# Kernel tuning notes

Measured on AMD Instinct MI355X. Metric: run time of the kernel, lower is better.

Reference implementation:

```python
import jax, jax.numpy as jnp
import numpy as np

B, S, D_IN, Z, D_OUT = 4, 2048, 4096, 1024, 4096
LN_EPS = 1e-5


def _ln(h, g, b):
    # LayerNorm over last axis (matches nn.LayerNorm(z_size))
    m = jnp.mean(h, axis=-1, keepdims=True)
    v = jnp.var(h, axis=-1, keepdims=True)
    return (h - m) * jax.lax.rsqrt(v + LN_EPS) * g + b


def setup_inputs() -> dict:
    key = jax.random.key(0)
    ks = jax.random.split(key, 8)
    s = 0.02  # init_weights uniform range
    return {
        "x": jax.random.normal(ks[0], (B, S, D_IN), jnp.float32),
        "epsilon": jax.random.normal(ks[1], (B, S, Z), jnp.float32),
        "W1": jax.random.uniform(ks[2], (Z, D_IN), jnp.float32, -s, s),
        "b1": jnp.zeros((Z,), jnp.float32),
        "g1": jnp.ones((Z,), jnp.float32),
        "be1": jnp.zeros((Z,), jnp.float32),
        "W2": jax.random.uniform(ks[3], (Z, Z), jnp.float32, -s, s),
        "b2": jnp.zeros((Z,), jnp.float32),
        "g2": jnp.ones((Z,), jnp.float32),
        "be2": jnp.zeros((Z,), jnp.float32),
        "Wmu": jax.random.uniform(ks[4], (Z, Z), jnp.float32, -s, s),
        "bmu": jnp.zeros((Z,), jnp.float32),
        "Wls": jax.random.uniform(ks[5], (Z, Z), jnp.float32, -s, s),
        "bls": jnp.zeros((Z,), jnp.float32),
        "Wzw": jax.random.uniform(ks[6], (D_OUT, D_OUT + Z), jnp.float32, -s, s),
        "bzw": jnp.zeros((D_OUT,), jnp.float32),
    }


def reference(x, epsilon, W1, b1, g1, be1, W2, b2, g2, be2,
              Wmu, bmu, Wls, bls, Wzw, bzw):
    # fc: Linear -> LayerNorm -> Tanh, twice
    h = jnp.tanh(_ln(jnp.einsum('bsd,zd->bsz', x, W1) + b1, g1, be1))
    h = jnp.tanh(_ln(jnp.einsum('bsz,yz->bsy', h, W2) + b2, g2, be2))
    mu = jnp.einsum('bsz,yz->bsy', h, Wmu) + bmu
    logsigma = jnp.einsum('bsz,yz->bsy', h, Wls) + bls
    std = jnp.exp(0.5 * logsigma)
    z = epsilon * std + mu                    # reparameterization
    z = jnp.concatenate([z, x], axis=2)       # [B,S,Z+D_IN]
    out = jnp.einsum('bsc,oc->bso', jnp.tanh(z), Wzw) + bzw
    return (out, mu, std)
```

## Files before the change

### kernel.cpp

```cpp
#include <hip/hip_runtime.h>
#include <cstdint>

typedef unsigned short u16;
typedef __bf16 bf16x8 __attribute__((ext_vector_type(8)));
typedef float f32x4 __attribute__((ext_vector_type(4)));

#define M_TOT 8192
#define D_IN  4096
#define Z_DIM 1024
#define D_OUT 4096
#define K_CAT 5120

struct alignas(8) u16x4 { u16 x, y, z, w; };

__device__ __forceinline__ u16 to_bf16(float f) {
    union { float f; uint32_t u; } v; v.f = f;
    uint32_t u = v.u;
    uint32_t r = (u + 0x7FFFu + ((u >> 16) & 1u)) >> 16;
    return (u16)r;
}

__device__ __forceinline__ void async_load16(const void* g, void* l) {
    __builtin_amdgcn_global_load_lds(
        (const __attribute__((address_space(1))) void*)g,
        (__attribute__((address_space(3))) void*)l,
        16, 0, 0);
}

__global__ __launch_bounds__(256)
void gemm_bt(const u16* __restrict__ A,
             const u16* __restrict__ Bw0, const u16* __restrict__ Bw1,
             const float* __restrict__ bias0, const float* __restrict__ bias1,
             float* __restrict__ C0, float* __restrict__ C1,
             int M, int N, int K)
{
    const u16*  Bw   = blockIdx.z ? Bw1   : Bw0;
    const float* bias = blockIdx.z ? bias1 : bias0;
    float*       C    = blockIdx.z ? C1    : C0;

    __shared__ u16 As[128 * 32];
    __shared__ u16 Bs[128 * 32];

    const int tid  = threadIdx.x;
    const int wave = tid >> 6;
    const int lane = tid & 63;
    const int m0 = blockIdx.y * 128;
    const int n0 = blockIdx.x * 128;
    const int wm = (wave & 1) * 64;
    const int wn = (wave >> 1) * 64;

    const int srow = wave * 32 + (lane >> 2);
    const int scol = (((lane & 3) ^ ((srow >> 1) & 3))) * 8;
    const long long a_off = (long long)(m0 + srow) * K + scol;
    const long long b_off = (long long)(n0 + srow) * K + scol;

    const int fr = lane & 15;
    const int fq = lane >> 4;
    const int rc = (fq ^ ((fr >> 1) & 3)) * 8;

    f32x4 acc[4][4] = {};

    for (int k0 = 0; k0 < K; k0 += 32) {
        async_load16(A  + a_off + k0,            &As[(wave * 32 +  0) * 32]);
        async_load16(A  + a_off + k0 + 16LL * K, &As[(wave * 32 + 16) * 32]);
        async_load16(Bw + b_off + k0,            &Bs[(wave * 32 +  0) * 32]);
        async_load16(Bw + b_off + k0 + 16LL * K, &Bs[(wave * 32 + 16) * 32]);
        __syncthreads();

        bf16x8 af[4], bf[4];
        #pragma unroll
        for (int i = 0; i < 4; i++)
            af[i] = *(const bf16x8*)&As[(wm + i * 16 + fr) * 32 + rc];
        #pragma unroll
        for (int i = 0; i < 4; i++)
            bf[i] = *(const bf16x8*)&Bs[(wn + i * 16 + fr) * 32 + rc];

        #pragma unroll
        for (int mi = 0; mi < 4; mi++)
            #pragma unroll
            for (int ni = 0; ni < 4; ni++)
                acc[mi][ni] = __builtin_amdgcn_mfma_f32_16x16x32_bf16(
                    af[mi], bf[ni], acc[mi][ni], 0, 0, 0);
        __syncthreads();
    }

    #pragma unroll
    for (int ni = 0; ni < 4; ni++) {
        const int col = n0 + wn + ni * 16 + fr;
        const float bv = bias[col];
        #pragma unroll
        for (int mi = 0; mi < 4; mi++) {
            const int row = m0 + wm + mi * 16 + fq * 4;
            float* cp = C + (long long)row * N + col;
            #pragma unroll
            for (int r = 0; r < 4; r++)
                cp[(long long)r * N] = acc[mi][ni][r] + bv;
        }
    }
}


#define BAR() do { asm volatile("" ::: "memory"); \
                   __builtin_amdgcn_s_barrier(); \
                   asm volatile("" ::: "memory"); } while (0)

#define STAGE_A(buf, h, kt_) do { if ((kt_) < nt) {                            \
    const u16* g_ = Ag + (long long)(h) * hstep + ((long long)(kt_) << 6);     \
    async_load16(g_,      &lds16[(buf) * 32768 + (h) * 8192        + wave * 512]); \
    async_load16(g_ + 32, &lds16[(buf) * 32768 + (h) * 8192 + 4096 + wave * 512]); \
  } } while (0)

#define STAGE_B(buf, h, kt_) do { if ((kt_) < nt) {                            \
    const u16* g_ = Bg + (long long)(h) * hstep + ((long long)(kt_) << 6);     \
    async_load16(g_,      &lds16[16384 + (buf) * 32768 + (h) * 8192        + wave * 512]); \
    async_load16(g_ + 32, &lds16[16384 + (buf) * 32768 + (h) * 8192 + 4096 + wave * 512]); \
  } } while (0)

#define LOAD_AF(buf, mbase)                                                    \
    _Pragma("unroll")                                                          \
    for (int mi_ = 0; mi_ < 4; ++mi_) {                                        \
      _Pragma("unroll")                                                        \
      for (int ks_ = 0; ks_ < 2; ++ks_)                                        \
        af[mi_][ks_] = *(const bf16x8*)&lds16[(buf) * 32768 + a_rd             \
                                              + ks_ * 4096 + ((mbase) + mi_) * 512]; \
    }

#define LOAD_B(dst, buf, nbase)                                                \
    _Pragma("unroll")                                                          \
    for (int ni_ = 0; ni_ < 2; ++ni_) {                                        \
      _Pragma("unroll")                                                        \
      for (int ks_ = 0; ks_ < 2; ++ks_)                                        \
        dst[ni_][ks_] = *(const bf16x8*)&lds16[(buf) * 32768 + b_rd            \
                                               + ks_ * 4096 + ((nbase) + ni_) * 512]; \
    }

#define MMA_Q(bfx, mo, no) do {                                                \
    __builtin_amdgcn_s_setprio(1);                                             \
    _Pragma("unroll")                                                          \
    for (int mi_ = 0; mi_ < 4; ++mi_) {                                        \
      _Pragma("unroll")                                                        \
      for (int ni_ = 0; ni_ < 2; ++ni_) {                                      \
        _Pragma("unroll")                                                      \
        for (int ks_ = 0; ks_ < 2; ++ks_)                                      \
          acc[(mo) + mi_][(no) + ni_] = __builtin_amdgcn_mfma_f32_16x16x32_bf16( \
              af[mi_][ks_], bfx[ni_][ks_], acc[(mo) + mi_][(no) + ni_], 0, 0, 0); \
      }                                                                        \
    }                                                                          \
    __builtin_amdgcn_s_setprio(0);                                             \
  } while (0)

#define TILE(b, kt_) do {                                                      \
                                            \
    LOAD_AF(b, 0);                                                             \
    LOAD_B(bf0, b, 0);                                                         \
    STAGE_A((b) ^ 1, 0, (kt_) + 1);                                            \
    BAR();                                                                     \
    MMA_Q(bf0, 0, 0);                                                          \
    BAR();                                                                     \
                                            \
    LOAD_B(bf1, b, 2);                                                         \
    STAGE_A((b) ^ 1, 1, (kt_) + 1);                                            \
    BAR();                                                                     \
    MMA_Q(bf1, 0, 2);                                                          \
    BAR();                                                                     \
     \
    LOAD_AF(b, 4);                                                             \
    STAGE_B(b, 0, (kt_) + 2);                                                  \
    BAR();                                                                     \
    MMA_Q(bf0, 4, 0);                                                          \
    BAR();                                                                     \
                                      \
    STAGE_B(b, 1, (kt_) + 2);                                                  \
    if ((kt_) + 2 < nt) { asm volatile("s_waitcnt vmcnt(4)" ::: "memory"); }   \
    else                { asm volatile("s_waitcnt vmcnt(0)" ::: "memory"); }   \
    BAR();                                                                     \
    MMA_Q(bf1, 4, 2);                                                          \
    BAR();                                                                     \
  } while (0)

__global__ __launch_bounds__(512)
void gemm256(const u16* __restrict__ A,
             const u16* __restrict__ Bw0, const u16* __restrict__ Bw1,
             const float* __restrict__ bias0, const float* __restrict__ bias1,
             float* __restrict__ C0, float* __restrict__ C1,
             int M, int N, int K)
{
    const u16*   Bw   = blockIdx.z ? Bw1   : Bw0;
    const float* bias = blockIdx.z ? bias1 : bias0;
    float*       C    = blockIdx.z ? C1    : C0;

    __shared__ u16 lds16[65536];

    const int tid  = threadIdx.x;
    const int wave = tid >> 6;
    const int lane = tid & 63;
    const int fr   = lane & 15;
    const int fq   = lane >> 4;
    const int wm   = (wave >> 2) * 128;
    const int wn   = (wave & 3) * 64;

    const int nwg  = (int)(gridDim.x * gridDim.y);
    const int bid0 = (int)(blockIdx.y * gridDim.x + blockIdx.x);
    const int bid  = (bid0 & 7) * (nwg >> 3) + (bid0 >> 3);
    const int n0   = (bid % (int)gridDim.x) * 256;
    const int m0   = (bid / (int)gridDim.x) * 256;

    const int nt = K >> 6;

    const int csrc = (tid & 3) ^ ((tid >> 4) & 2);
    const u16* Ag = A  + (long long)(m0 + (tid >> 2)) * K + csrc * 8;
    const u16* Bg = Bw + (long long)(n0 + (tid >> 2)) * K + csrc * 8;
    const long long hstep = 128LL * K;

    const int swz  = (fq * 8) ^ ((fr & 8) << 1);
    const int a_rd = (wave >> 2) * 8192 + fr * 32 + swz;
    const int b_rd = 16384 + ((wave & 3) >> 1) * 8192
                   + ((wave & 1) * 64 + fr) * 32 + swz;

    f32x4 acc[8][4] = {};
    bf16x8 af[4][2], bf0[2][2], bf1[2][2];

    STAGE_B(0, 0, 0);
    STAGE_B(0, 1, 0);
    STAGE_A(0, 0, 0);
    STAGE_A(0, 1, 0);
    STAGE_B(1, 0, 1);
    STAGE_B(1, 1, 1);
    asm volatile("s_waitcnt vmcnt(4)" ::: "memory");
    BAR();

    #pragma unroll 1
    for (int kt = 0; kt < nt; kt += 2) {
        TILE(0, kt);
        TILE(1, kt + 1);
    }

    #pragma unroll
    for (int ni = 0; ni < 4; ++ni) {
        const int col = n0 + wn + ni * 16 + fr;
        const float bv = bias[col];
        #pragma unroll
        for (int mi = 0; mi < 8; ++mi) {
            const int row = m0 + wm + mi * 16 + fq * 4;
            float* cp = C + (long long)row * N + col;
            #pragma unroll
            for (int r = 0; r < 4; ++r)
                cp[(long long)r * N] = acc[mi][ni][r] + bv;
        }
    }
}

#undef BAR
#undef STAGE_A
#undef STAGE_B
#undef LOAD_AF
#undef LOAD_B
#undef MMA_Q
#undef TILE

__global__ __launch_bounds__(256)
void ln_tanh_kernel(const float* __restrict__ in, const float* __restrict__ g,
                    const float* __restrict__ be, u16* __restrict__ out)
{
    const int row = blockIdx.x;
    const int t = threadIdx.x;
    const float4 v = ((const float4*)(in + (long long)row * 1024))[t];
    float s  = v.x + v.y + v.z + v.w;
    float s2 = v.x * v.x + v.y * v.y + v.z * v.z + v.w * v.w;
    #pragma unroll
    for (int off = 32; off > 0; off >>= 1) {
        s  += __shfl_down(s,  off);
        s2 += __shfl_down(s2, off);
    }
    __shared__ float red[8];
    if ((t & 63) == 0) { red[t >> 6] = s; red[4 + (t >> 6)] = s2; }
    __syncthreads();
    s  = red[0] + red[1] + red[2] + red[3];
    s2 = red[4] + red[5] + red[6] + red[7];
    const float mean = s * (1.0f / 1024.0f);
    const float inv  = rsqrtf(s2 * (1.0f / 1024.0f) - mean * mean + 1e-5f);
    const float4 gg = ((const float4*)g)[t];
    const float4 bb = ((const float4*)be)[t];
    u16x4 o;
    o.x = to_bf16(tanhf((v.x - mean) * inv * gg.x + bb.x));
    o.y = to_bf16(tanhf((v.y - mean) * inv * gg.y + bb.y));
    o.z = to_bf16(tanhf((v.z - mean) * inv * gg.z + bb.z));
    o.w = to_bf16(tanhf((v.w - mean) * inv * gg.w + bb.w));
    ((u16x4*)(out + (long long)row * 1024))[t] = o;
}

__global__ __launch_bounds__(256)
void prep_x_kernel(const float* __restrict__ x, u16* __restrict__ xb,
                   u16* __restrict__ zc)
{
    const long long i = (long long)blockIdx.x * 256 + threadIdx.x;
    const float4 v = ((const float4*)x)[i];
    u16x4 b;
    b.x = to_bf16(v.x); b.y = to_bf16(v.y); b.z = to_bf16(v.z); b.w = to_bf16(v.w);
    ((u16x4*)xb)[i] = b;
    const long long flat = i * 4;
    const long long row = flat >> 12;
    const int col = (int)(flat & 4095);
    u16x4 tq;
    tq.x = to_bf16(tanhf(v.x)); tq.y = to_bf16(tanhf(v.y));
    tq.z = to_bf16(tanhf(v.z)); tq.w = to_bf16(tanhf(v.w));
    *(u16x4*)(zc + row * (long long)K_CAT + 1024 + col) = tq;
}

__global__ __launch_bounds__(256)
void reparam_kernel(const float* __restrict__ mu, float* __restrict__ lsstd,
                    const float* __restrict__ eps, u16* __restrict__ zc)
{
    const long long row = blockIdx.x;
    const int c = threadIdx.x * 4;
    const long long idx = row * 1024 + c;
    const float4 m = *(const float4*)(mu + idx);
    const float4 l = *(const float4*)(lsstd + idx);
    const float4 e = *(const float4*)(eps + idx);
    float4 sd;
    sd.x = expf(0.5f * l.x); sd.y = expf(0.5f * l.y);
    sd.z = expf(0.5f * l.z); sd.w = expf(0.5f * l.w);
    *(float4*)(lsstd + idx) = sd;
    u16x4 t;
    t.x = to_bf16(tanhf(e.x * sd.x + m.x));
    t.y = to_bf16(tanhf(e.y * sd.y + m.y));
    t.z = to_bf16(tanhf(e.z * sd.z + m.z));
    t.w = to_bf16(tanhf(e.w * sd.w + m.w));
    *(u16x4*)(zc + row * (long long)K_CAT + c) = t;
}

__global__ __launch_bounds__(256)
void cvt_kernel(const float* __restrict__ src, u16* __restrict__ dst, long long n4)
{
    const long long i = (long long)blockIdx.x * 256 + threadIdx.x;
    if (i >= n4) return;
    const float4 v = ((const float4*)src)[i];
    u16x4 b;
    b.x = to_bf16(v.x); b.y = to_bf16(v.y); b.z = to_bf16(v.z); b.w = to_bf16(v.w);
    ((u16x4*)dst)[i] = b;
}

__global__ __launch_bounds__(256)
void cvt4_kernel(const float* __restrict__ s0, u16* __restrict__ d0,
                 const float* __restrict__ s1, u16* __restrict__ d1,
                 const float* __restrict__ s2, u16* __restrict__ d2,
                 const float* __restrict__ s3, u16* __restrict__ d3)
{
    long long i = (long long)blockIdx.x * 256 + threadIdx.x;
    const float* s; u16* d;
    if (i < 1048576)      { s = s0; d = d0; }
    else if (i < 1310720) { s = s1; d = d1; i -= 1048576; }
    else if (i < 1572864) { s = s2; d = d2; i -= 1310720; }
    else                  { s = s3; d = d3; i -= 1572864; }
    const float4 v = ((const float4*)s)[i];
    u16x4 b;
    b.x = to_bf16(v.x); b.y = to_bf16(v.y); b.z = to_bf16(v.z); b.w = to_bf16(v.w);
    ((u16x4*)d)[i] = b;
}

extern "C" void kernel_launch(void* const* d_in, const int* in_sizes, int n_in,
                              void* d_out, int out_size, void* d_ws, size_t ws_size,
                              hipStream_t stream)
{
    const float* x   = (const float*)d_in[0];
    const float* eps = (const float*)d_in[1];
    const float* W1  = (const float*)d_in[2];
    const float* b1  = (const float*)d_in[3];
    const float* g1  = (const float*)d_in[4];
    const float* be1 = (const float*)d_in[5];
    const float* W2  = (const float*)d_in[6];
    const float* b2  = (const float*)d_in[7];
    const float* g2  = (const float*)d_in[8];
    const float* be2 = (const float*)d_in[9];
    const float* Wmu = (const float*)d_in[10];
    const float* bmu = (const float*)d_in[11];
    const float* Wls = (const float*)d_in[12];
    const float* bls = (const float*)d_in[13];
    const float* Wzw = (const float*)d_in[14];
    const float* bzw = (const float*)d_in[15];

    float* out  = (float*)d_out;
    float* mu   = out + (long long)M_TOT * D_OUT;
    float* std_ = mu  + (long long)M_TOT * Z_DIM;

    char* ws = (char*)d_ws;
    u16*   xb   = (u16*)(ws);
    u16*   zc   = (u16*)(ws +  67108864);
    u16*   h1   = (u16*)(ws + 150994944);
    u16*   h2   = (u16*)(ws + 167772160);
    float* pre  = (float*)(ws + 184549376);
    u16*   W1b  = (u16*)(ws + 218103808);
    u16*   W2b  = (u16*)(ws + 226492416);
    u16*   Wmub = (u16*)(ws + 228589568);
    u16*   Wlsb = (u16*)(ws + 230686720);
    u16*   Wzwb = (u16*)(ws);

    cvt4_kernel<<<7168, 256, 0, stream>>>(W1, W1b, W2, W2b, Wmu, Wmub, Wls, Wlsb);

    prep_x_kernel<<<32768, 256, 0, stream>>>(x, xb, zc);

    gemm_bt<<<dim3(8, 64, 1), 256, 0, stream>>>(xb, W1b, W1b, b1, b1, pre, pre,
                                                M_TOT, Z_DIM, D_IN);
    ln_tanh_kernel<<<8192, 256, 0, stream>>>(pre, g1, be1, h1);

    cvt_kernel<<<20480, 256, 0, stream>>>(Wzw, Wzwb, 5242880);

    gemm_bt<<<dim3(8, 64, 1), 256, 0, stream>>>(h1, W2b, W2b, b2, b2, pre, pre,
                                                M_TOT, Z_DIM, Z_DIM);
    ln_tanh_kernel<<<8192, 256, 0, stream>>>(pre, g2, be2, h2);

    gemm256<<<dim3(4, 32, 2), 512, 0, stream>>>(h2, Wmub, Wlsb, bmu, bls, mu, std_,
                                                M_TOT, Z_DIM, Z_DIM);

    reparam_kernel<<<8192, 256, 0, stream>>>(mu, std_, eps, zc);

    gemm256<<<dim3(16, 32, 1), 512, 0, stream>>>(zc, Wzwb, Wzwb, bzw, bzw, out, out,
                                                 M_TOT, D_OUT, K_CAT);
}
```

Measured before the change: 930.7 us.

## Restructure GEMM main loop into k-split register pipeline with fewer barriers

Reorganises the inner tile of the 256x256 GEMM so each step splits K into two halves. Per wave it loads 4 A fragments and 4 B fragments and issues 16 MFMAs per group, and it prefetches the next tile's first fragments before the last MMA group. Barriers drop from eight per tile to two. Global-to-LDS staging for both A and B now targets the other buffer one tile ahead, replacing the previous B-two-tiles-ahead scheme, and waits with vmcnt(0). This cuts barrier stalls and LDS read latency exposure, but it uses more fragment registers and shortens the global prefetch distance.

```diff
diff --git a/kernel.cpp b/kernel.cpp
--- a/kernel.cpp
+++ b/kernel.cpp
@@ -116,65 +116,53 @@
     async_load16(g_ + 32, &lds16[16384 + (buf) * 32768 + (h) * 8192 + 4096 + wave * 512]); \
   } } while (0)
 
-#define LOAD_AF(buf, mbase)                                                    \
+#define R_AF(dst, buf, mbase, ks)                                              \
     _Pragma("unroll")                                                          \
-    for (int mi_ = 0; mi_ < 4; ++mi_) {                                        \
-      _Pragma("unroll")                                                        \
-      for (int ks_ = 0; ks_ < 2; ++ks_)                                        \
-        af[mi_][ks_] = *(const bf16x8*)&lds16[(buf) * 32768 + a_rd             \
-                                              + ks_ * 4096 + ((mbase) + mi_) * 512]; \
-    }
-
-#define LOAD_B(dst, buf, nbase)                                                \
+    for (int mi_ = 0; mi_ < 4; ++mi_)                                          \
+      dst[mi_] = *(const bf16x8*)&lds16[(buf) * 32768 + a_rd                   \
+                                        + (ks) * 4096 + ((mbase) + mi_) * 512];
+
+#define R_BF(dst, buf, ks)                                                     \
     _Pragma("unroll")                                                          \
-    for (int ni_ = 0; ni_ < 2; ++ni_) {                                        \
-      _Pragma("unroll")                                                        \
-      for (int ks_ = 0; ks_ < 2; ++ks_)                                        \
-        dst[ni_][ks_] = *(const bf16x8*)&lds16[(buf) * 32768 + b_rd            \
-                                               + ks_ * 4096 + ((nbase) + ni_) * 512]; \
-    }
-
-#define MMA_Q(bfx, mo, no) do {                                                \
+    for (int ni_ = 0; ni_ < 4; ++ni_)                                          \
+      dst[ni_] = *(const bf16x8*)&lds16[(buf) * 32768 + b_rd                   \
+                                        + (ks) * 4096 + ni_ * 512];
+
+#define MMA16(mo, afv, bfv) do {                                               \
     __builtin_amdgcn_s_setprio(1);                                             \
     _Pragma("unroll")                                                          \
     for (int mi_ = 0; mi_ < 4; ++mi_) {                                        \
       _Pragma("unroll")                                                        \
-      for (int ni_ = 0; ni_ < 2; ++ni_) {                                      \
-        _Pragma("unroll")                                                      \
-        for (int ks_ = 0; ks_ < 2; ++ks_)                                      \
-          acc[(mo) + mi_][(no) + ni_] = __builtin_amdgcn_mfma_f32_16x16x32_bf16( \
-              af[mi_][ks_], bfx[ni_][ks_], acc[(mo) + mi_][(no) + ni_], 0, 0, 0); \
-      }                                                                        \
+      for (int ni_ = 0; ni_ < 4; ++ni_)                                        \
+        acc[(mo) + mi_][ni_] = __builtin_amdgcn_mfma_f32_16x16x32_bf16(        \
+            afv[mi_], bfv[ni_], acc[(mo) + mi_][ni_], 0, 0, 0);                \
     }                                                                          \
     __builtin_amdgcn_s_setprio(0);                                             \
   } while (0)
 
 #define TILE(b, kt_) do {                                                      \
-                                            \
-    LOAD_AF(b, 0);                                                             \
-    LOAD_B(bf0, b, 0);                                                         \
+                       \
+    R_AF(afB, b, 4, 0);                                                        \
     STAGE_A((b) ^ 1, 0, (kt_) + 1);                                            \
+    STAGE_A((b) ^ 1, 1, (kt_) + 1);                                            \
+    MMA16(0, afA, bfA);                                                        \
+                \
+    R_AF(afC, b, 0, 1);                                                        \
+    R_BF(bfB, b, 1);                                                           \
+    STAGE_B((b) ^ 1, 0, (kt_) + 1);                                            \
+    STAGE_B((b) ^ 1, 1, (kt_) + 1);                                            \
+    MMA16(4, afB, bfA);                                                        \
+            \
+    R_AF(afD, b, 4, 1);                                                        \
+    MMA16(0, afC, bfB);                                                        \
+    asm volatile("s_waitcnt vmcnt(0)" ::: "memory");                           \
     BAR();                                                                     \
-    MMA_Q(bf0, 0, 0);                                                          \
-    BAR();                                                                     \
-                                            \
-    LOAD_B(bf1, b, 2);                                                         \
-    STAGE_A((b) ^ 1, 1, (kt_) + 1);                                            \
-    BAR();                                                                     \
-    MMA_Q(bf1, 0, 2);                                                          \
-    BAR();                                                                     \
-     \
-    LOAD_AF(b, 4);                                                             \
-    STAGE_B(b, 0, (kt_) + 2);                                                  \
-    BAR();                                                                     \
-    MMA_Q(bf0, 4, 0);                                                          \
-    BAR();                                                                     \
-                                      \
-    STAGE_B(b, 1, (kt_) + 2);                                                  \
-    if ((kt_) + 2 < nt) { asm volatile("s_waitcnt vmcnt(4)" ::: "memory"); }   \
-    else                { asm volatile("s_waitcnt vmcnt(0)" ::: "memory"); }   \
-    BAR();                                                                     \
-    MMA_Q(bf1, 4, 2);                                                          \
+            \
+    if ((kt_) + 1 < nt) {                                                      \
+      R_AF(afA, (b) ^ 1, 0, 0);                                                \
+      R_BF(bfA, (b) ^ 1, 0);                                                   \
+    }                                                                          \
+    MMA16(4, afD, bfB);                                                        \
     BAR();                                                                     \
   } while (0)
 
@@ -218,16 +206,16 @@
                    + ((wave & 1) * 64 + fr) * 32 + swz;
 
     f32x4 acc[8][4] = {};
-    bf16x8 af[4][2], bf0[2][2], bf1[2][2];
-
+    bf16x8 afA[4], afB[4], afC[4], afD[4], bfA[4], bfB[4];
+
+    STAGE_A(0, 0, 0);
+    STAGE_A(0, 1, 0);
     STAGE_B(0, 0, 0);
     STAGE_B(0, 1, 0);
-    STAGE_A(0, 0, 0);
-    STAGE_A(0, 1, 0);
-    STAGE_B(1, 0, 1);
-    STAGE_B(1, 1, 1);
-    asm volatile("s_waitcnt vmcnt(4)" ::: "memory");
+    asm volatile("s_waitcnt vmcnt(0)" ::: "memory");
     BAR();
+    R_AF(afA, 0, 0, 0);
+    R_BF(bfA, 0, 0);
 
     #pragma unroll 1
     for (int kt = 0; kt < nt; kt += 2) {
@@ -253,9 +241,9 @@
 #undef BAR
 #undef STAGE_A
 #undef STAGE_B
-#undef LOAD_AF
-#undef LOAD_B
-#undef MMA_Q
+#undef R_AF
+#undef R_BF
+#undef MMA16
 #undef TILE
 
 __global__ __launch_bounds__(256)
```

Result: slower. 1.153 ms (+23.9%).

## Switch gemm256 to 32x32x16 MFMA and fuse exp into logsigma epilogue

Applied to the files above, without the earlier changes.

Rewrites the 256x256 GEMM inner loop to use 32x32x16 bf16 MFMA tiles instead of 16x16x32. The LDS fragment reads, swizzle and register layout change to match, and the B fragments for the next tile are prefetched across iterations. The larger instruction should give more math per LDS read and fewer instructions per tile. The exp(0.5*x) for std moves into the GEMM epilogue, so reparam no longer reads and rewrites that buffer. The new LDS read pattern may cause bank conflicts, and the epilogue stores become strided by row.

```diff
diff --git a/kernel.cpp b/kernel.cpp
--- a/kernel.cpp
+++ b/kernel.cpp
@@ -4,6 +4,7 @@
 typedef unsigned short u16;
 typedef __bf16 bf16x8 __attribute__((ext_vector_type(8)));
 typedef float f32x4 __attribute__((ext_vector_type(4)));
+typedef float f32x16 __attribute__((ext_vector_type(16)));
 
 #define M_TOT 8192
 #define D_IN  4096
@@ -116,65 +117,67 @@
     async_load16(g_ + 32, &lds16[16384 + (buf) * 32768 + (h) * 8192 + 4096 + wave * 512]); \
   } } while (0)
 
-#define LOAD_AF(buf, mbase)                                                    \
+#define R32A(dst, buf, mp, sp)                                                 \
     _Pragma("unroll")                                                          \
-    for (int mi_ = 0; mi_ < 4; ++mi_) {                                        \
+    for (int mi_ = 0; mi_ < 2; ++mi_) {                                        \
       _Pragma("unroll")                                                        \
-      for (int ks_ = 0; ks_ < 2; ++ks_)                                        \
-        af[mi_][ks_] = *(const bf16x8*)&lds16[(buf) * 32768 + a_rd             \
-                                              + ks_ * 4096 + ((mbase) + mi_) * 512]; \
-    }
-
-#define LOAD_B(dst, buf, nbase)                                                \
+      for (int si_ = 0; si_ < 2; ++si_)                                        \
+        dst[mi_][si_] = *(const bf16x8*)&lds16[(buf) * 32768 + a_rd            \
+            + (sp) * 4096 + ((mp) * 2 + mi_) * 1024 + (si_ ^ rb) * 16];        \
+    }
+
+#define R32B(dst, buf, sp)                                                     \
     _Pragma("unroll")                                                          \
     for (int ni_ = 0; ni_ < 2; ++ni_) {                                        \
       _Pragma("unroll")                                                        \
-      for (int ks_ = 0; ks_ < 2; ++ks_)                                        \
-        dst[ni_][ks_] = *(const bf16x8*)&lds16[(buf) * 32768 + b_rd            \
-                                               + ks_ * 4096 + ((nbase) + ni_) * 512]; \
-    }
-
-#define MMA_Q(bfx, mo, no) do {                                                \
+      for (int si_ = 0; si_ < 2; ++si_)                                        \
+        dst[ni_][si_] = *(const bf16x8*)&lds16[(buf) * 32768 + b_rd            \
+            + (sp) * 4096 + ni_ * 1024 + (si_ ^ rb) * 16];                     \
+    }
+
+#define MMA32(mp, afv, bfv) do {                                               \
     __builtin_amdgcn_s_setprio(1);                                             \
     _Pragma("unroll")                                                          \
-    for (int mi_ = 0; mi_ < 4; ++mi_) {                                        \
+    for (int si_ = 0; si_ < 2; ++si_) {                                        \
       _Pragma("unroll")                                                        \
-      for (int ni_ = 0; ni_ < 2; ++ni_) {                                      \
+      for (int mi_ = 0; mi_ < 2; ++mi_) {                                      \
         _Pragma("unroll")                                                      \
-        for (int ks_ = 0; ks_ < 2; ++ks_)                                      \
-          acc[(mo) + mi_][(no) + ni_] = __builtin_amdgcn_mfma_f32_16x16x32_bf16( \
-              af[mi_][ks_], bfx[ni_][ks_], acc[(mo) + mi_][(no) + ni_], 0, 0, 0); \
+        for (int ni_ = 0; ni_ < 2; ++ni_)                                      \
+          acc[(mp) * 2 + mi_][ni_] = __builtin_amdgcn_mfma_f32_32x32x16_bf16(  \
+              afv[mi_][si_], bfv[ni_][si_], acc[(mp) * 2 + mi_][ni_], 0, 0, 0);\
       }                                                                        \
     }                                                                          \
     __builtin_amdgcn_s_setprio(0);                                             \
   } while (0)
 
 #define TILE(b, kt_) do {                                                      \
-                                            \
-    LOAD_AF(b, 0);                                                             \
-    LOAD_B(bf0, b, 0);                                                         \
+                               \
+    R32A(afE, b, 0, 0);                                                        \
     STAGE_A((b) ^ 1, 0, (kt_) + 1);                                            \
     BAR();                                                                     \
-    MMA_Q(bf0, 0, 0);                                                          \
-    BAR();                                                                     \
-                                            \
-    LOAD_B(bf1, b, 2);                                                         \
+    MMA32(0, afE, bf01);                                                       \
+    BAR();                                                                     \
+         \
+    R32A(afO, b, 1, 0);                                                        \
+    R32B(bf23, b, 1);                                                          \
     STAGE_A((b) ^ 1, 1, (kt_) + 1);                                            \
     BAR();                                                                     \
-    MMA_Q(bf1, 0, 2);                                                          \
-    BAR();                                                                     \
-     \
-    LOAD_AF(b, 4);                                                             \
+    MMA32(1, afO, bf01);                                                       \
+    BAR();                                                                     \
+                          \
+    R32A(afE, b, 0, 1);                                                        \
     STAGE_B(b, 0, (kt_) + 2);                                                  \
     BAR();                                                                     \
-    MMA_Q(bf0, 4, 0);                                                          \
-    BAR();                                                                     \
-                                      \
+    MMA32(0, afE, bf23);                                                       \
+    BAR();                                                                     \
+            \
+    R32A(afO, b, 1, 1);                                                        \
     STAGE_B(b, 1, (kt_) + 2);                                                  \
     if ((kt_) + 2 < nt) { asm volatile("s_waitcnt vmcnt(4)" ::: "memory"); }   \
     else                { asm volatile("s_waitcnt vmcnt(0)" ::: "memory"); }   \
     BAR();                                                                     \
-    MMA_Q(bf1, 4, 2);                                                          \
+    R32B(bf01, (b) ^ 1, 0);                                                    \
+    MMA32(1, afO, bf23);                                                       \
     BAR();                                                                     \
   } while (0)
 
@@ -183,19 +186,21 @@
              const u16* __restrict__ Bw0, const u16* __restrict__ Bw1,
              const float* __restrict__ bias0, const float* __restrict__ bias1,
              float* __restrict__ C0, float* __restrict__ C1,
-             int M, int N, int K)
+             int M, int N, int K, int expls)
 {
     const u16*   Bw   = blockIdx.z ? Bw1   : Bw0;
     const float* bias = blockIdx.z ? bias1 : bias0;
     float*       C    = blockIdx.z ? C1    : C0;
+    const int doexp   = expls && blockIdx.z;
 
     __shared__ u16 lds16[65536];
 
     const int tid  = threadIdx.x;
     const int wave = tid >> 6;
     const int lane = tid & 63;
-    const int fr   = lane & 15;
-    const int fq   = lane >> 4;
+    const int l31  = lane & 31;
+    const int lh   = lane >> 5;
+    const int rb   = (l31 >> 3) & 1;
     const int wm   = (wave >> 2) * 128;
     const int wn   = (wave & 3) * 64;
 
@@ -212,13 +217,12 @@
     const u16* Bg = Bw + (long long)(n0 + (tid >> 2)) * K + csrc * 8;
     const long long hstep = 128LL * K;
 
-    const int swz  = (fq * 8) ^ ((fr & 8) << 1);
-    const int a_rd = (wave >> 2) * 8192 + fr * 32 + swz;
+    const int a_rd = (wave >> 2) * 8192 + l31 * 32 + lh * 8;
     const int b_rd = 16384 + ((wave & 3) >> 1) * 8192
-                   + ((wave & 1) * 64 + fr) * 32 + swz;
-
-    f32x4 acc[8][4] = {};
-    bf16x8 af[4][2], bf0[2][2], bf1[2][2];
+                   + ((wave & 1) * 64 + l31) * 32 + lh * 8;
+
+    f32x16 acc[4][2] = {};
+    bf16x8 afE[2][2], afO[2][2], bf01[2][2], bf23[2][2];
 
     STAGE_B(0, 0, 0);
     STAGE_B(0, 1, 0);
@@ -228,6 +232,7 @@
     STAGE_B(1, 1, 1);
     asm volatile("s_waitcnt vmcnt(4)" ::: "memory");
     BAR();
+    R32B(bf01, 0, 0);
 
     #pragma unroll 1
     for (int kt = 0; kt < nt; kt += 2) {
@@ -236,16 +241,18 @@
     }
 
     #pragma unroll
-    for (int ni = 0; ni < 4; ++ni) {
-        const int col = n0 + wn + ni * 16 + fr;
+    for (int n32 = 0; n32 < 2; ++n32) {
+        const int col = n0 + wn + n32 * 32 + l31;
         const float bv = bias[col];
         #pragma unroll
-        for (int mi = 0; mi < 8; ++mi) {
-            const int row = m0 + wm + mi * 16 + fq * 4;
-            float* cp = C + (long long)row * N + col;
+        for (int m32 = 0; m32 < 4; ++m32) {
             #pragma unroll
-            for (int r = 0; r < 4; ++r)
-                cp[(long long)r * N] = acc[mi][ni][r] + bv;
+            for (int r = 0; r < 16; ++r) {
+                const int row = m0 + wm + m32 * 32 + (r & 3) + 8 * (r >> 2) + 4 * lh;
+                float v = acc[m32][n32][r] + bv;
+                if (doexp) v = expf(0.5f * v);
+                C[(long long)row * N + col] = v;
+            }
         }
     }
 }
@@ -253,9 +260,9 @@
 #undef BAR
 #undef STAGE_A
 #undef STAGE_B
-#undef LOAD_AF
-#undef LOAD_B
-#undef MMA_Q
+#undef R32A
+#undef R32B
+#undef MMA32
 #undef TILE
 
 __global__ __launch_bounds__(256)
@@ -308,19 +315,15 @@
 }
 
 __global__ __launch_bounds__(256)
-void reparam_kernel(const float* __restrict__ mu, float* __restrict__ lsstd,
+void reparam_kernel(const float* __restrict__ mu, const float* __restrict__ stdv,
                     const float* __restrict__ eps, u16* __restrict__ zc)
 {
     const long long row = blockIdx.x;
     const int c = threadIdx.x * 4;
     const long long idx = row * 1024 + c;
     const float4 m = *(const float4*)(mu + idx);
-    const float4 l = *(const float4*)(lsstd + idx);
+    const float4 sd = *(const float4*)(stdv + idx);
     const float4 e = *(const float4*)(eps + idx);
-    float4 sd;
-    sd.x = expf(0.5f * l.x); sd.y = expf(0.5f * l.y);
-    sd.z = expf(0.5f * l.z); sd.w = expf(0.5f * l.w);
-    *(float4*)(lsstd + idx) = sd;
     u16x4 t;
     t.x = to_bf16(tanhf(e.x * sd.x + m.x));
     t.y = to_bf16(tanhf(e.y * sd.y + m.y));
@@ -410,10 +413,10 @@
     ln_tanh_kernel<<<8192, 256, 0, stream>>>(pre, g2, be2, h2);
 
     gemm256<<<dim3(4, 32, 2), 512, 0, stream>>>(h2, Wmub, Wlsb, bmu, bls, mu, std_,
-                                                M_TOT, Z_DIM, Z_DIM);
+                                                M_TOT, Z_DIM, Z_DIM, 1);
 
     reparam_kernel<<<8192, 256, 0, stream>>>(mu, std_, eps, zc);
 
     gemm256<<<dim3(16, 32, 1), 512, 0, stream>>>(zc, Wzwb, Wzwb, bzw, bzw, out, out,
-                                                 M_TOT, D_OUT, K_CAT);
-}
+                                                 M_TOT, D_OUT, K_CAT, 0);
+}
```

Measured after the change: 943.6 us. About the same (+1.4%).
